# Performance work log

Hardware: AMD Instinct MI355X
Metric: run time of the kernel (lower is better)

Reference implementation:

```python
import jax, jax.numpy as jnp
import numpy as np

B, T, I, H = 128, 1024, 256, 512


def setup_inputs() -> dict:
    key = jax.random.key(0)
    ks = jax.random.split(key, 7)
    s_in = 1.0 / np.sqrt(I + H)  # torch Linear default init scale
    inp = {
        "x": jax.random.normal(ks[0], (B, T, I), dtype=jnp.float32),
        "Wz": jax.random.uniform(ks[1], (I + H, H), jnp.float32, -s_in, s_in),
        "bz": jax.random.uniform(ks[2], (H,), jnp.float32, -s_in, s_in),
        "Wr": jax.random.uniform(ks[3], (I + H, H), jnp.float32, -s_in, s_in),
        "br": jax.random.uniform(ks[4], (H,), jnp.float32, -s_in, s_in),
        "Wh": jax.random.uniform(ks[5], (I + H, H), jnp.float32, -s_in, s_in),
        "bh": jax.random.uniform(ks[6], (H,), jnp.float32, -s_in, s_in),
    }
    return inp


def reference(x, Wz, bz, Wr, br, Wh, bh):
    # x: [B, T, I]; custom GRU cell, h0 = zeros. Note the (nonstandard)
    # blend h = (1-z)*h + z*h_cand, exactly as in the torch source.
    batch, hidden = x.shape[0], Wz.shape[1]

    def step(h, x_t):
        comb = jnp.concatenate([x_t, h], axis=1)          # [B, I+H]
        z = jax.nn.sigmoid(comb @ Wz + bz)                # [B, H]
        r = jax.nn.sigmoid(comb @ Wr + br)                # [B, H]
        comb2 = jnp.concatenate([x_t, r * h], axis=1)     # [B, I+H]
        h_cand = jnp.tanh(comb2 @ Wh + bh)                # [B, H]
        h_new = (1.0 - z) * h + z * h_cand
        return h_new, h_new

    h0 = jnp.zeros((batch, hidden), dtype=x.dtype)
    _, ys = jax.lax.scan(step, h0, jnp.swapaxes(x, 0, 1))  # ys: [T, B, H]
    return jnp.swapaxes(ys, 0, 1)                          # [B, T, H]
```

## Files before the change

kernel.cpp:

```cpp
#include <hip/hip_runtime.h>
#include <math.h>

#define BB 128
#define TT 1024
#define II 256
#define HH 512
#define KK 768

typedef __attribute__((ext_vector_type(8))) short short8v;
typedef __attribute__((ext_vector_type(4))) float float4v;
typedef __attribute__((ext_vector_type(4))) unsigned int uint4v;

#define BARS_OFF   0
#define BARS_SZ    32768
#define WFRAG_OFF  BARS_SZ
#define WFRAG_SZ   (96 * 24 * 64 * 16)
#define GS_OFF     (WFRAG_OFF + WFRAG_SZ)
#define GS_STRIDE  65536
#define WS_NEED    ((size_t)GS_OFF + 8 * GS_STRIDE)

#define NT_MAIN 320

__device__ __forceinline__ unsigned short bf16_rne(float f) {
    unsigned u = __builtin_bit_cast(unsigned, f);
    unsigned r = u + 0x7FFFu + ((u >> 16) & 1u);
    return (unsigned short)(r >> 16);
}
__device__ __forceinline__ void cp16(void* lds, const void* g) {
    __builtin_amdgcn_global_load_lds(
        (const __attribute__((address_space(1))) unsigned*)g,
        (__attribute__((address_space(3))) unsigned*)lds, 16, 0, 0);
}
__device__ __forceinline__ float sigmoid_fast(float v) {
    return __builtin_amdgcn_rcpf(1.f + __expf(-v));
}
__device__ __forceinline__ float tanh_fast(float v) {
    const float e = __expf(2.f * v);
    return 1.f - 2.f * __builtin_amdgcn_rcpf(e + 1.f);
}

#define MFMA __builtin_amdgcn_mfma_f32_16x16x32_bf16

__global__ void repack_w(const float* __restrict__ Wz, const float* __restrict__ Wr,
                         const float* __restrict__ Wh, short8v* __restrict__ wB) {
    const int ntAll = blockIdx.x;
    const int w = threadIdx.x >> 6, l = threadIdx.x & 63;
    const float* W; int n0;
    if (ntAll < 32)      { W = Wz; n0 = ntAll * 16; }
    else if (ntAll < 64) { W = Wr; n0 = (ntAll - 32) * 16; }
    else                 { W = Wh; n0 = (ntAll - 64) * 16; }
    const int n = n0 + (l & 15);
    for (int kt = w; kt < 24; kt += 4) {
        const int k0 = kt * 32 + (l >> 4) * 8;
        short8v f;
        #pragma unroll
        for (int j = 0; j < 8; ++j)
            f[j] = (short)bf16_rne(W[(size_t)(k0 + j) * HH + n]);
        wB[((size_t)ntAll * 24 + kt) * 64 + l] = f;
    }
}

__global__ __launch_bounds__(NT_MAIN, 1) void gru_mfma(
    const float* __restrict__ x,
    const float* __restrict__ bz, const float* __restrict__ br,
    const float* __restrict__ bh,
    float* __restrict__ out,
    const short8v* __restrict__ wB,
    char* __restrict__ gsBase,
    unsigned* __restrict__ bars)
{
    __shared__ short8v bx1[4][8][64];
    __shared__ short8v bx2[2][8][64];
    __shared__ short8v xF[2][8][64];
    __shared__ float4v red1[4][4][64];
    __shared__ float4v red2[2][4][64];
    __shared__ float rhA[16][33];
    __shared__ float hL[16][33];

    const int tid = threadIdx.x;
    const int w = tid >> 6, l = tid & 63;
    const int g = blockIdx.x & 7, s = blockIdx.x >> 3;
    const int m_ = l & 15, kg = l >> 4;

    char* gs = gsBase + (size_t)g * GS_STRIDE;
    short8v* hFrag  = (short8v*)gs;
    short8v* rhFrag = hFrag + 16 * 64;
    unsigned* flagBase = bars + (size_t)g * 16 * 64;

    short8v wh1[4][4];
    short8v wh2[2][4];
    if (w < 4) {
        const int ownNt = (w < 2) ? (2 * s + w) : (32 + 2 * s + (w - 2));
        for (int i = 0; i < 8; ++i)
            cp16(&bx1[w][i][0], wB + ((size_t)ownNt * 24 + i) * 64 + l);
        if (w < 2)
            for (int i = 0; i < 8; ++i)
                cp16(&bx2[w][i][0], wB + ((size_t)(64 + 2 * s + w) * 24 + i) * 64 + l);
        #pragma unroll
        for (int T = 0; T < 4; ++T) {
            const int nt = (T < 2) ? (2 * s + T) : (32 + 2 * s + (T - 2));
            #pragma unroll
            for (int q = 0; q < 4; ++q)
                wh1[T][q] = wB[((size_t)nt * 24 + 8 + 4 * w + q) * 64 + l];
        }
        #pragma unroll
        for (int n2 = 0; n2 < 2; ++n2)
            #pragma unroll
            for (int q = 0; q < 4; ++q)
                wh2[n2][q] = wB[((size_t)(64 + 2 * s + n2) * 24 + 8 + 4 * w + q) * 64 + l];
    }
    const float bias1 = (w < 2) ? bz[s * 32 + w * 16 + m_]
                    : (w < 4)  ? br[s * 32 + (w - 2) * 16 + m_] : 0.f;
    const float bias2 = (w < 2) ? bh[s * 32 + w * 16 + m_] : 0.f;

    for (int idx = tid; idx < 16 * 33; idx += NT_MAIN) ((float*)hL)[idx] = 0.f;

    for (int slot = tid; slot < 512; slot += NT_MAIN) {
        const int kt = slot >> 6, ll = slot & 63;
        const float* xp = x + (size_t)(g * 16 + (ll & 15)) * (TT * II)
                            + kt * 32 + (ll >> 4) * 8;
        const float4 v0 = *(const float4*)xp;
        const float4 v1 = *(const float4*)(xp + 4);
        short8v f;
        f[0] = (short)bf16_rne(v0.x); f[1] = (short)bf16_rne(v0.y);
        f[2] = (short)bf16_rne(v0.z); f[3] = (short)bf16_rne(v0.w);
        f[4] = (short)bf16_rne(v1.x); f[5] = (short)bf16_rne(v1.y);
        f[6] = (short)bf16_rne(v1.z); f[7] = (short)bf16_rne(v1.w);
        xF[0][kt][ll] = f;
    }
    __syncthreads();

    float4 xv[16];

    for (int t = 0; t < TT; ++t) {
        const int xb = t & 1;

        float4v ax0 = {0.f, 0.f, 0.f, 0.f}, ax1 = ax0;
        if (w < 4) {
            #pragma unroll
            for (int kt = 0; kt < 8; kt += 2) {
                ax0 = MFMA(xF[xb][kt][l],     bx1[w][kt][l],     ax0, 0, 0, 0);
                ax1 = MFMA(xF[xb][kt + 1][l], bx1[w][kt + 1][l], ax1, 0, 0, 0);
            }
        } else if (t + 1 < TT) {
            #pragma unroll
            for (int i = 0; i < 8; ++i) {
                const float* xp = x + (size_t)(g * 16 + m_) * (TT * II)
                                    + (size_t)(t + 1) * II + i * 32 + kg * 8;
                xv[2 * i]     = *(const float4*)xp;
                xv[2 * i + 1] = *(const float4*)(xp + 4);
            }
        }

        if (w < 4) {
            if (l < 8) {
                const unsigned* fp = flagBase + (4 * w + (l >> 1)) * 64 + (l & 1) * 8;
                while (__hip_atomic_load(fp, __ATOMIC_RELAXED,
                                         __HIP_MEMORY_SCOPE_AGENT) < (unsigned)t)
                    __builtin_amdgcn_s_sleep(1);
            }
            uint4v u0, u1, u2, u3;
            const short8v* hp = hFrag + (size_t)(4 * w) * 64 + l;
            asm volatile("global_load_dwordx4 %0, %1, off sc1" : "=v"(u0) : "v"(hp)       : "memory");
            asm volatile("global_load_dwordx4 %0, %1, off sc1" : "=v"(u1) : "v"(hp +  64) : "memory");
            asm volatile("global_load_dwordx4 %0, %1, off sc1" : "=v"(u2) : "v"(hp + 128) : "memory");
            asm volatile("global_load_dwordx4 %0, %1, off sc1" : "=v"(u3) : "v"(hp + 192) : "memory");
            asm volatile("s_waitcnt vmcnt(0)" ::: "memory");
            __builtin_amdgcn_sched_barrier(0);
            const short8v hf0 = __builtin_bit_cast(short8v, u0);
            const short8v hf1 = __builtin_bit_cast(short8v, u1);
            const short8v hf2 = __builtin_bit_cast(short8v, u2);
            const short8v hf3 = __builtin_bit_cast(short8v, u3);
            float4v h0 = {0.f,0.f,0.f,0.f}, h1 = h0, h2 = h0, h3 = h0;
            #pragma unroll
            for (int q = 0; q < 4; ++q) {
                const short8v a = (q == 0) ? hf0 : (q == 1) ? hf1 : (q == 2) ? hf2 : hf3;
                h0 = MFMA(a, wh1[0][q], h0, 0, 0, 0);
                h1 = MFMA(a, wh1[1][q], h1, 0, 0, 0);
                h2 = MFMA(a, wh1[2][q], h2, 0, 0, 0);
                h3 = MFMA(a, wh1[3][q], h3, 0, 0, 0);
            }
            red1[0][w][l] = h0; red1[1][w][l] = h1;
            red1[2][w][l] = h2; red1[3][w][l] = h3;
        }
        __syncthreads();

        float zreg[4];
        if (w < 4) {
            float4v s1v = ax0 + ax1 + red1[w][0][l] + red1[w][1][l]
                                  + red1[w][2][l] + red1[w][3][l];
            #pragma unroll
            for (int r = 0; r < 4; ++r) {
                const float sg = sigmoid_fast(s1v[r] + bias1);
                if (w < 2) zreg[r] = sg;
                else rhA[kg * 4 + r][(w - 2) * 16 + m_] =
                         sg * hL[kg * 4 + r][(w - 2) * 16 + m_];
            }
        }
        if (w == 2 || w == 3) {
            asm volatile("s_waitcnt lgkmcnt(0)" ::: "memory");
            __builtin_amdgcn_sched_barrier(0);
            const bool mine = (w == 2) ? (l < 32) : (l >= 32);
            if (mine) {
                short8v f;
                #pragma unroll
                for (int j = 0; j < 8; ++j)
                    f[j] = (short)bf16_rne(rhA[m_][kg * 8 + j]);
                const uint4v u = __builtin_bit_cast(uint4v, f);
                short8v* dp = rhFrag + (size_t)s * 64 + l;
                asm volatile("global_store_dwordx4 %0, %1, off sc1" :: "v"(dp), "v"(u) : "memory");
            }
            asm volatile("s_waitcnt vmcnt(0)" ::: "memory");
            if (w == 2 && l == 0)
                __hip_atomic_store(flagBase + s * 64 + 16, (unsigned)(t + 1),
                                   __ATOMIC_RELAXED, __HIP_MEMORY_SCOPE_AGENT);
            if (w == 3 && l == 32)
                __hip_atomic_store(flagBase + s * 64 + 24, (unsigned)(t + 1),
                                   __ATOMIC_RELAXED, __HIP_MEMORY_SCOPE_AGENT);
        }
        if (w == 4) {
            asm volatile("s_waitcnt vmcnt(0)" ::: "memory");
            if (t + 1 < TT) {
                #pragma unroll
                for (int i = 0; i < 8; ++i) {
                    const float4 v0 = xv[2 * i], v1 = xv[2 * i + 1];
                    short8v f;
                    f[0] = (short)bf16_rne(v0.x); f[1] = (short)bf16_rne(v0.y);
                    f[2] = (short)bf16_rne(v0.z); f[3] = (short)bf16_rne(v0.w);
                    f[4] = (short)bf16_rne(v1.x); f[5] = (short)bf16_rne(v1.y);
                    f[6] = (short)bf16_rne(v1.z); f[7] = (short)bf16_rne(v1.w);
                    xF[xb ^ 1][i][l] = f;
                }
            }
            if (t > 0) {
                float* op = out + (size_t)(g * 16 + m_) * (TT * HH)
                                + (size_t)(t - 1) * HH + s * 32 + kg * 8;
                float4 o0, o1;
                o0.x = hL[m_][kg * 8 + 0]; o0.y = hL[m_][kg * 8 + 1];
                o0.z = hL[m_][kg * 8 + 2]; o0.w = hL[m_][kg * 8 + 3];
                o1.x = hL[m_][kg * 8 + 4]; o1.y = hL[m_][kg * 8 + 5];
                o1.z = hL[m_][kg * 8 + 6]; o1.w = hL[m_][kg * 8 + 7];
                *(float4*)op = o0;
                *(float4*)(op + 4) = o1;
            }
        }

        float4v cx0 = {0.f,0.f,0.f,0.f}, cx1 = cx0;
        if (w < 2) {
            #pragma unroll
            for (int kt = 0; kt < 8; kt += 2) {
                cx0 = MFMA(xF[xb][kt][l],     bx2[w][kt][l],     cx0, 0, 0, 0);
                cx1 = MFMA(xF[xb][kt + 1][l], bx2[w][kt + 1][l], cx1, 0, 0, 0);
            }
        }

        if (w < 4) {
            if (l < 8) {
                const unsigned* fp = flagBase + (4 * w + (l >> 1)) * 64 + 16 + (l & 1) * 8;
                while (__hip_atomic_load(fp, __ATOMIC_RELAXED,
                                         __HIP_MEMORY_SCOPE_AGENT) < (unsigned)(t + 1))
                    __builtin_amdgcn_s_sleep(1);
            }
            uint4v u0, u1, u2, u3;
            const short8v* rp = rhFrag + (size_t)(4 * w) * 64 + l;
            asm volatile("global_load_dwordx4 %0, %1, off sc1" : "=v"(u0) : "v"(rp)       : "memory");
            asm volatile("global_load_dwordx4 %0, %1, off sc1" : "=v"(u1) : "v"(rp +  64) : "memory");
            asm volatile("global_load_dwordx4 %0, %1, off sc1" : "=v"(u2) : "v"(rp + 128) : "memory");
            asm volatile("global_load_dwordx4 %0, %1, off sc1" : "=v"(u3) : "v"(rp + 192) : "memory");
            asm volatile("s_waitcnt vmcnt(0)" ::: "memory");
            __builtin_amdgcn_sched_barrier(0);
            const short8v rf0 = __builtin_bit_cast(short8v, u0);
            const short8v rf1 = __builtin_bit_cast(short8v, u1);
            const short8v rf2 = __builtin_bit_cast(short8v, u2);
            const short8v rf3 = __builtin_bit_cast(short8v, u3);
            float4v c0 = {0.f,0.f,0.f,0.f}, c1 = c0;
            #pragma unroll
            for (int q = 0; q < 4; ++q) {
                const short8v a = (q == 0) ? rf0 : (q == 1) ? rf1 : (q == 2) ? rf2 : rf3;
                c0 = MFMA(a, wh2[0][q], c0, 0, 0, 0);
                c1 = MFMA(a, wh2[1][q], c1, 0, 0, 0);
            }
            red2[0][w][l] = c0; red2[1][w][l] = c1;
        }
        __syncthreads();

        if (w < 2) {
            float4v s2v = cx0 + cx1 + red2[w][0][l] + red2[w][1][l]
                                  + red2[w][2][l] + red2[w][3][l];
            #pragma unroll
            for (int r = 0; r < 4; ++r) {
                const int row = kg * 4 + r;
                const int cl = w * 16 + m_;
                const float hc = tanh_fast(s2v[r] + bias2);
                const float ho = hL[row][cl];
                hL[row][cl] = (1.f - zreg[r]) * ho + zreg[r] * hc;
            }
            asm volatile("s_waitcnt lgkmcnt(0)" ::: "memory");
            __builtin_amdgcn_sched_barrier(0);
            const bool mine = (w == 0) ? (l < 32) : (l >= 32);
            if (mine) {
                short8v f;
                #pragma unroll
                for (int j = 0; j < 8; ++j)
                    f[j] = (short)bf16_rne(hL[m_][kg * 8 + j]);
                const uint4v u = __builtin_bit_cast(uint4v, f);
                short8v* dp = hFrag + (size_t)s * 64 + l;
                asm volatile("global_store_dwordx4 %0, %1, off sc1" :: "v"(dp), "v"(u) : "memory");
            }
            asm volatile("s_waitcnt vmcnt(0)" ::: "memory");
            if (w == 0 && l == 0)
                __hip_atomic_store(flagBase + s * 64 + 0, (unsigned)(t + 1),
                                   __ATOMIC_RELAXED, __HIP_MEMORY_SCOPE_AGENT);
            if (w == 1 && l == 32)
                __hip_atomic_store(flagBase + s * 64 + 8, (unsigned)(t + 1),
                                   __ATOMIC_RELAXED, __HIP_MEMORY_SCOPE_AGENT);
        }
    }

    __syncthreads();
    if (w == 4) {
        float* op = out + (size_t)(g * 16 + m_) * (TT * HH)
                        + (size_t)(TT - 1) * HH + s * 32 + kg * 8;
        float4 o0, o1;
        o0.x = hL[m_][kg * 8 + 0]; o0.y = hL[m_][kg * 8 + 1];
        o0.z = hL[m_][kg * 8 + 2]; o0.w = hL[m_][kg * 8 + 3];
        o1.x = hL[m_][kg * 8 + 4]; o1.y = hL[m_][kg * 8 + 5];
        o1.z = hL[m_][kg * 8 + 6]; o1.w = hL[m_][kg * 8 + 7];
        *(float4*)op = o0;
        *(float4*)(op + 4) = o1;
    }
}

#define NWG_FB 64
#define NTHR_FB 512
__global__ __launch_bounds__(NTHR_FB, 1) void gru_rowsplit(
    const float* __restrict__ x,
    const float* __restrict__ Wz, const float* __restrict__ bz,
    const float* __restrict__ Wr, const float* __restrict__ br,
    const float* __restrict__ Wh, const float* __restrict__ bh,
    float* __restrict__ out)
{
    __shared__ float comb_i [KK][2];
    __shared__ float comb2_i[KK][2];
    __shared__ float z_s[2][HH];
    __shared__ float red1[8][257];
    __shared__ float red2[24][129];

    const int tid  = threadIdx.x;
    const int row0 = blockIdx.x * 2;
    const int kh = tid >> 8;
    const int t1 = tid & 255;
    const int n1 = t1 * 4;
    const float* __restrict__ w1 =
        ((n1 < HH) ? (Wz + n1) : (Wr + (n1 - HH))) + (size_t)(kh * 384) * HH;
    const int kq = tid >> 7;
    const int t2 = tid & 127;
    const int n2 = t2 * 4;
    const float* __restrict__ w2 = Wh + n2 + (size_t)(kq * 192) * HH;

    float b1[4], b2[4];
    #pragma unroll
    for (int j = 0; j < 4; ++j) {
        b1[j] = (n1 + j < HH) ? bz[n1 + j] : br[n1 + j - HH];
        b2[j] = bh[n2 + j];
    }
    for (int idx = tid; idx < HH * 2; idx += NTHR_FB)
        comb_i[II + (idx >> 1)][idx & 1] = 0.f;
    __syncthreads();

    for (int t = 0; t < TT; ++t) {
        {
            const int r = tid >> 8, k = tid & 255;
            const float v = x[(size_t)(row0 + r) * (TT * II) + (size_t)t * II + k];
            comb_i [k][r] = v;
            comb2_i[k][r] = v;
        }
        __syncthreads();
        float a00=0,a01=0,a02=0,a03=0,a10=0,a11=0,a12=0,a13=0;
        {
            const int kb = kh * 384;
            #pragma unroll 8
            for (int k = 0; k < 384; ++k) {
                const float4 w = *(const float4*)(w1 + (size_t)k * HH);
                const float2 a = *(const float2*)&comb_i[kb + k][0];
                a00 += a.x*w.x; a01 += a.x*w.y; a02 += a.x*w.z; a03 += a.x*w.w;
                a10 += a.y*w.x; a11 += a.y*w.y; a12 += a.y*w.z; a13 += a.y*w.w;
            }
        }
        if (kh == 1) {
            red1[0][t1]=a00; red1[1][t1]=a01; red1[2][t1]=a02; red1[3][t1]=a03;
            red1[4][t1]=a10; red1[5][t1]=a11; red1[6][t1]=a12; red1[7][t1]=a13;
        }
        __syncthreads();
        if (kh == 0) {
            float accv[2][4] = {{a00,a01,a02,a03},{a10,a11,a12,a13}};
            #pragma unroll
            for (int r = 0; r < 2; ++r) {
                #pragma unroll
                for (int j = 0; j < 4; ++j) {
                    const int n = n1 + j;
                    const float v = accv[r][j] + red1[r*4+j][t1] + b1[j];
                    const float sg = 1.f / (1.f + __expf(-v));
                    if (n < HH) z_s[r][n] = sg;
                    else {
                        const int nh = n - HH;
                        comb2_i[II + nh][r] = sg * comb_i[II + nh][r];
                    }
                }
            }
        }
        __syncthreads();
        float c00=0,c01=0,c02=0,c03=0,c10=0,c11=0,c12=0,c13=0;
        {
            const int kb = kq * 192;
            #pragma unroll 8
            for (int k = 0; k < 192; ++k) {
                const float4 w = *(const float4*)(w2 + (size_t)k * HH);
                const float2 a = *(const float2*)&comb2_i[kb + k][0];
                c00 += a.x*w.x; c01 += a.x*w.y; c02 += a.x*w.z; c03 += a.x*w.w;
                c10 += a.y*w.x; c11 += a.y*w.y; c12 += a.y*w.z; c13 += a.y*w.w;
            }
        }
        if (kq > 0) {
            const int base = (kq - 1) * 8;
            red2[base+0][t2]=c00; red2[base+1][t2]=c01;
            red2[base+2][t2]=c02; red2[base+3][t2]=c03;
            red2[base+4][t2]=c10; red2[base+5][t2]=c11;
            red2[base+6][t2]=c12; red2[base+7][t2]=c13;
        }
        __syncthreads();
        if (kq == 0) {
            float accv[2][4] = {{c00,c01,c02,c03},{c10,c11,c12,c13}};
            #pragma unroll
            for (int r = 0; r < 2; ++r) {
                float hn4[4];
                #pragma unroll
                for (int j = 0; j < 4; ++j) {
                    const int n = n2 + j;
                    const int jj = r * 4 + j;
                    const float v = accv[r][j] + red2[jj][t2] + red2[8+jj][t2]
                                  + red2[16+jj][t2] + b2[j];
                    const float hc = tanhf(v);
                    const float zv = z_s[r][n];
                    const float ho = comb_i[II + n][r];
                    const float hn = (1.f - zv) * ho + zv * hc;
                    comb_i[II + n][r] = hn;
                    hn4[j] = hn;
                }
                *(float4*)&out[(size_t)(row0 + r) * (TT * HH) + (size_t)t * HH + n2] =
                    make_float4(hn4[0], hn4[1], hn4[2], hn4[3]);
            }
        }
        __syncthreads();
    }
}

extern "C" void kernel_launch(void* const* d_in, const int* in_sizes, int n_in,
                              void* d_out, int out_size, void* d_ws, size_t ws_size,
                              hipStream_t stream) {
    const float* x  = (const float*)d_in[0];
    const float* Wz = (const float*)d_in[1];
    const float* bz = (const float*)d_in[2];
    const float* Wr = (const float*)d_in[3];
    const float* br = (const float*)d_in[4];
    const float* Wh = (const float*)d_in[5];
    const float* bh = (const float*)d_in[6];
    float* out = (float*)d_out;

    if (ws_size < WS_NEED) {
        gru_rowsplit<<<NWG_FB, NTHR_FB, 0, stream>>>(x, Wz, bz, Wr, br, Wh, bh, out);
        return;
    }

    char* ws = (char*)d_ws;
    unsigned* bars = (unsigned*)(ws + BARS_OFF);
    short8v*  wB   = (short8v*)(ws + WFRAG_OFF);
    char*     gs   = ws + GS_OFF;

    hipMemsetAsync(bars, 0, BARS_SZ, stream);
    hipMemsetAsync(gs, 0, 8 * (size_t)GS_STRIDE, stream);
    repack_w<<<96, 256, 0, stream>>>(Wz, Wr, Wh, wB);
    gru_mfma<<<128, NT_MAIN, 0, stream>>>(x, bz, br, bh, out, wB, gs, bars);
}
```

Baseline: 4.569 ms.

## Probe at runtime for shared-L2 locality and use sc0 cache-scope polling when safe

Adds a startup probe in which the 16 workgroups of each batch group exchange flags using sc0-scoped loads and stores, checking whether they can see each other's writes. If every member of the group passes, the per-step flag polling, fragment stores and fragment loads switch from sc1 (device-scope) to sc0 cache policy and spin without s_sleep. The goal is lower latency on the two cross-workgroup exchanges in every timestep. It risks relying on coherence behaviour that only the probe confirms, which could go wrong if workgroups land on different XCDs. It also adds probe setup cost and doubles the barrier workspace.

```diff
diff --git a/kernel.cpp b/kernel.cpp
--- a/kernel.cpp
+++ b/kernel.cpp
@@ -12,7 +12,7 @@
 typedef __attribute__((ext_vector_type(4))) unsigned int uint4v;
 
 #define BARS_OFF   0
-#define BARS_SZ    32768
+#define BARS_SZ    65536
 #define WFRAG_OFF  BARS_SZ
 #define WFRAG_SZ   (96 * 24 * 64 * 16)
 #define GS_OFF     (WFRAG_OFF + WFRAG_SZ)
@@ -37,6 +37,22 @@
 __device__ __forceinline__ float tanh_fast(float v) {
     const float e = __expf(2.f * v);
     return 1.f - 2.f * __builtin_amdgcn_rcpf(e + 1.f);
+}
+__device__ __forceinline__ unsigned poll_ld(const unsigned* p, bool fast) {
+    unsigned v;
+    if (fast) asm volatile("global_load_dword %0, %1, off sc0\n\ts_waitcnt vmcnt(0)"
+                           : "=v"(v) : "v"(p) : "memory");
+    else      asm volatile("global_load_dword %0, %1, off sc1\n\ts_waitcnt vmcnt(0)"
+                           : "=v"(v) : "v"(p) : "memory");
+    return v;
+}
+__device__ __forceinline__ void frag_st16(void* p, uint4v u, bool fast) {
+    if (fast) asm volatile("global_store_dwordx4 %0, %1, off sc0" :: "v"(p), "v"(u) : "memory");
+    else      asm volatile("global_store_dwordx4 %0, %1, off sc1" :: "v"(p), "v"(u) : "memory");
+}
+__device__ __forceinline__ void flag_pub(unsigned* p, unsigned v, bool fast) {
+    if (fast) asm volatile("global_store_dword %0, %1, off sc0" :: "v"(p), "v"(v) : "memory");
+    else      __hip_atomic_store(p, v, __ATOMIC_RELAXED, __HIP_MEMORY_SCOPE_AGENT);
 }
 
 #define MFMA __builtin_amdgcn_mfma_f32_16x16x32_bf16
@@ -76,6 +92,7 @@
     __shared__ float4v red2[2][4][64];
     __shared__ float rhA[16][33];
     __shared__ float hL[16][33];
+    __shared__ int fastSh;
 
     const int tid = threadIdx.x;
     const int w = tid >> 6, l = tid & 63;
@@ -85,7 +102,8 @@
     char* gs = gsBase + (size_t)g * GS_STRIDE;
     short8v* hFrag  = (short8v*)gs;
     short8v* rhFrag = hFrag + 16 * 64;
-    unsigned* flagBase = bars + (size_t)g * 16 * 64;
+    unsigned* flagBase  = bars + (size_t)g * 16 * 64;
+    unsigned* probeBase = bars + 8192 + (size_t)g * 16 * 64;
 
     short8v wh1[4][4];
     short8v wh2[2][4];
@@ -115,6 +133,45 @@
 
     for (int idx = tid; idx < 16 * 33; idx += NT_MAIN) ((float*)hL)[idx] = 0.f;
 
+    if (w == 0) {
+        int okAll = 1;
+        for (int round = 1; round <= 4; ++round) {
+            if (l == 0) {
+                unsigned* pp = probeBase + s * 64;
+                asm volatile("global_store_dword %0, %1, off sc0\n\ts_waitcnt vmcnt(0)"
+                             :: "v"(pp), "v"((unsigned)round) : "memory");
+            }
+            bool seen = (l >= 16);
+            if (l < 16) {
+                const unsigned* pp = probeBase + l * 64;
+                const unsigned bound = (round == 1) ? 8192u : 2048u;
+                for (unsigned it = 0; it < bound; ++it) {
+                    unsigned v;
+                    asm volatile("global_load_dword %0, %1, off sc0\n\ts_waitcnt vmcnt(0)"
+                                 : "=v"(v) : "v"(pp) : "memory");
+                    if (v >= (unsigned)round) { seen = true; break; }
+                }
+            }
+            okAll &= (((unsigned long long)__ballot(seen) & 0xFFFFull) == 0xFFFFull) ? 1 : 0;
+        }
+        if (l == 0)
+            __hip_atomic_store(probeBase + s * 64 + 16, (unsigned)(1 + okAll),
+                               __ATOMIC_RELAXED, __HIP_MEMORY_SCOPE_AGENT);
+        bool good = (l >= 16);
+        if (l < 16) {
+            const unsigned* vp = probeBase + l * 64 + 16;
+            unsigned v;
+            for (;;) {
+                v = __hip_atomic_load(vp, __ATOMIC_RELAXED, __HIP_MEMORY_SCOPE_AGENT);
+                if (v != 0u) break;
+                __builtin_amdgcn_s_sleep(1);
+            }
+            good = (v == 2u);
+        }
+        if (l == 0)
+            fastSh = (((unsigned long long)__ballot(good) & 0xFFFFull) == 0xFFFFull) ? 1 : 0;
+    }
+
     for (int slot = tid; slot < 512; slot += NT_MAIN) {
         const int kt = slot >> 6, ll = slot & 63;
         const float* xp = x + (size_t)(g * 16 + (ll & 15)) * (TT * II)
@@ -129,6 +186,7 @@
         xF[0][kt][ll] = f;
     }
     __syncthreads();
+    const bool fast = (fastSh != 0);
 
     float4 xv[16];
 
@@ -155,16 +213,26 @@
         if (w < 4) {
             if (l < 8) {
                 const unsigned* fp = flagBase + (4 * w + (l >> 1)) * 64 + (l & 1) * 8;
-                while (__hip_atomic_load(fp, __ATOMIC_RELAXED,
-                                         __HIP_MEMORY_SCOPE_AGENT) < (unsigned)t)
-                    __builtin_amdgcn_s_sleep(1);
+                if (fast) { while (poll_ld(fp, true) < (unsigned)t) {} }
+                else {
+                    while (__hip_atomic_load(fp, __ATOMIC_RELAXED,
+                                             __HIP_MEMORY_SCOPE_AGENT) < (unsigned)t)
+                        __builtin_amdgcn_s_sleep(1);
+                }
             }
             uint4v u0, u1, u2, u3;
             const short8v* hp = hFrag + (size_t)(4 * w) * 64 + l;
-            asm volatile("global_load_dwordx4 %0, %1, off sc1" : "=v"(u0) : "v"(hp)       : "memory");
-            asm volatile("global_load_dwordx4 %0, %1, off sc1" : "=v"(u1) : "v"(hp +  64) : "memory");
-            asm volatile("global_load_dwordx4 %0, %1, off sc1" : "=v"(u2) : "v"(hp + 128) : "memory");
-            asm volatile("global_load_dwordx4 %0, %1, off sc1" : "=v"(u3) : "v"(hp + 192) : "memory");
+            if (fast) {
+                asm volatile("global_load_dwordx4 %0, %1, off sc0" : "=v"(u0) : "v"(hp)       : "memory");
+                asm volatile("global_load_dwordx4 %0, %1, off sc0" : "=v"(u1) : "v"(hp +  64) : "memory");
+                asm volatile("global_load_dwordx4 %0, %1, off sc0" : "=v"(u2) : "v"(hp + 128) : "memory");
+                asm volatile("global_load_dwordx4 %0, %1, off sc0" : "=v"(u3) : "v"(hp + 192) : "memory");
+            } else {
+                asm volatile("global_load_dwordx4 %0, %1, off sc1" : "=v"(u0) : "v"(hp)       : "memory");
+                asm volatile("global_load_dwordx4 %0, %1, off sc1" : "=v"(u1) : "v"(hp +  64) : "memory");
+                asm volatile("global_load_dwordx4 %0, %1, off sc1" : "=v"(u2) : "v"(hp + 128) : "memory");
+                asm volatile("global_load_dwordx4 %0, %1, off sc1" : "=v"(u3) : "v"(hp + 192) : "memory");
+            }
             asm volatile("s_waitcnt vmcnt(0)" ::: "memory");
             __builtin_amdgcn_sched_barrier(0);
             const short8v hf0 = __builtin_bit_cast(short8v, u0);
@@ -206,17 +274,11 @@
                 #pragma unroll
                 for (int j = 0; j < 8; ++j)
                     f[j] = (short)bf16_rne(rhA[m_][kg * 8 + j]);
-                const uint4v u = __builtin_bit_cast(uint4v, f);
-                short8v* dp = rhFrag + (size_t)s * 64 + l;
-                asm volatile("global_store_dwordx4 %0, %1, off sc1" :: "v"(dp), "v"(u) : "memory");
+                frag_st16(rhFrag + (size_t)s * 64 + l, __builtin_bit_cast(uint4v, f), fast);
             }
             asm volatile("s_waitcnt vmcnt(0)" ::: "memory");
-            if (w == 2 && l == 0)
-                __hip_atomic_store(flagBase + s * 64 + 16, (unsigned)(t + 1),
-                                   __ATOMIC_RELAXED, __HIP_MEMORY_SCOPE_AGENT);
-            if (w == 3 && l == 32)
-                __hip_atomic_store(flagBase + s * 64 + 24, (unsigned)(t + 1),
-                                   __ATOMIC_RELAXED, __HIP_MEMORY_SCOPE_AGENT);
+            if (w == 2 && l == 0)  flag_pub(flagBase + s * 64 + 16, (unsigned)(t + 1), fast);
+            if (w == 3 && l == 32) flag_pub(flagBase + s * 64 + 24, (unsigned)(t + 1), fast);
         }
         if (w == 4) {
             asm volatile("s_waitcnt vmcnt(0)" ::: "memory");
@@ -257,16 +319,26 @@
         if (w < 4) {
             if (l < 8) {
                 const unsigned* fp = flagBase + (4 * w + (l >> 1)) * 64 + 16 + (l & 1) * 8;
-                while (__hip_atomic_load(fp, __ATOMIC_RELAXED,
-                                         __HIP_MEMORY_SCOPE_AGENT) < (unsigned)(t + 1))
-                    __builtin_amdgcn_s_sleep(1);
+                if (fast) { while (poll_ld(fp, true) < (unsigned)(t + 1)) {} }
+                else {
+                    while (__hip_atomic_load(fp, __ATOMIC_RELAXED,
+                                             __HIP_MEMORY_SCOPE_AGENT) < (unsigned)(t + 1))
+                        __builtin_amdgcn_s_sleep(1);
+                }
             }
             uint4v u0, u1, u2, u3;
             const short8v* rp = rhFrag + (size_t)(4 * w) * 64 + l;
-            asm volatile("global_load_dwordx4 %0, %1, off sc1" : "=v"(u0) : "v"(rp)       : "memory");
-            asm volatile("global_load_dwordx4 %0, %1, off sc1" : "=v"(u1) : "v"(rp +  64) : "memory");
-            asm volatile("global_load_dwordx4 %0, %1, off sc1" : "=v"(u2) : "v"(rp + 128) : "memory");
-            asm volatile("global_load_dwordx4 %0, %1, off sc1" : "=v"(u3) : "v"(rp + 192) : "memory");
+            if (fast) {
+                asm volatile("global_load_dwordx4 %0, %1, off sc0" : "=v"(u0) : "v"(rp)       : "memory");
+                asm volatile("global_load_dwordx4 %0, %1, off sc0" : "=v"(u1) : "v"(rp +  64) : "memory");
+                asm volatile("global_load_dwordx4 %0, %1, off sc0" : "=v"(u2) : "v"(rp + 128) : "memory");
+                asm volatile("global_load_dwordx4 %0, %1, off sc0" : "=v"(u3) : "v"(rp + 192) : "memory");
+            } else {
+                asm volatile("global_load_dwordx4 %0, %1, off sc1" : "=v"(u0) : "v"(rp)       : "memory");
+                asm volatile("global_load_dwordx4 %0, %1, off sc1" : "=v"(u1) : "v"(rp +  64) : "memory");
+                asm volatile("global_load_dwordx4 %0, %1, off sc1" : "=v"(u2) : "v"(rp + 128) : "memory");
+                asm volatile("global_load_dwordx4 %0, %1, off sc1" : "=v"(u3) : "v"(rp + 192) : "memory");
+            }
             asm volatile("s_waitcnt vmcnt(0)" ::: "memory");
             __builtin_amdgcn_sched_barrier(0);
             const short8v rf0 = __builtin_bit_cast(short8v, u0);
@@ -303,17 +375,11 @@
                 #pragma unroll
                 for (int j = 0; j < 8; ++j)
                     f[j] = (short)bf16_rne(hL[m_][kg * 8 + j]);
-                const uint4v u = __builtin_bit_cast(uint4v, f);
-                short8v* dp = hFrag + (size_t)s * 64 + l;
-                asm volatile("global_store_dwordx4 %0, %1, off sc1" :: "v"(dp), "v"(u) : "memory");
+                frag_st16(hFrag + (size_t)s * 64 + l, __builtin_bit_cast(uint4v, f), fast);
             }
             asm volatile("s_waitcnt vmcnt(0)" ::: "memory");
-            if (w == 0 && l == 0)
-                __hip_atomic_store(flagBase + s * 64 + 0, (unsigned)(t + 1),
-                                   __ATOMIC_RELAXED, __HIP_MEMORY_SCOPE_AGENT);
-            if (w == 1 && l == 32)
-                __hip_atomic_store(flagBase + s * 64 + 8, (unsigned)(t + 1),
-                                   __ATOMIC_RELAXED, __HIP_MEMORY_SCOPE_AGENT);
+            if (w == 0 && l == 0)  flag_pub(flagBase + s * 64 + 0, (unsigned)(t + 1), fast);
+            if (w == 1 && l == 32) flag_pub(flagBase + s * 64 + 8, (unsigned)(t + 1), fast);
         }
     }
 
```

New measurement: 5.544 ms. 1.21x slower.

## Replace flag-based cross-block sync with epoch-tagged data messages

Applied to the files above, without the earlier changes.

Each published bf16 pair of the h and r*h fragments now carries its own epoch word in an 8-byte store. Consumers poll the data itself until every epoch reaches the step, which removes the separate flag arrays, the store-then-wait-then-flag sequence, and the flag spin loop. This cuts one global round trip per exchange. In exchange, message traffic doubles, each poll issues sixteen dwordx2 loads, and correctness relies on each 8-byte store being seen atomically.

```diff
diff --git a/kernel.cpp b/kernel.cpp
--- a/kernel.cpp
+++ b/kernel.cpp
@@ -10,12 +10,11 @@
 typedef __attribute__((ext_vector_type(8))) short short8v;
 typedef __attribute__((ext_vector_type(4))) float float4v;
 typedef __attribute__((ext_vector_type(4))) unsigned int uint4v;
-
-#define BARS_OFF   0
-#define BARS_SZ    32768
-#define WFRAG_OFF  BARS_SZ
+typedef __attribute__((ext_vector_type(2))) unsigned int uint2v;
+
+#define WFRAG_OFF  0
 #define WFRAG_SZ   (96 * 24 * 64 * 16)
-#define GS_OFF     (WFRAG_OFF + WFRAG_SZ)
+#define GS_OFF     WFRAG_SZ
 #define GS_STRIDE  65536
 #define WS_NEED    ((size_t)GS_OFF + 8 * GS_STRIDE)
 
@@ -38,6 +37,7 @@
     const float e = __expf(2.f * v);
     return 1.f - 2.f * __builtin_amdgcn_rcpf(e + 1.f);
 }
+__device__ __forceinline__ unsigned umin2(unsigned a, unsigned b) { return a < b ? a : b; }
 
 #define MFMA __builtin_amdgcn_mfma_f32_16x16x32_bf16
 
@@ -66,8 +66,7 @@
     const float* __restrict__ bh,
     float* __restrict__ out,
     const short8v* __restrict__ wB,
-    char* __restrict__ gsBase,
-    unsigned* __restrict__ bars)
+    char* __restrict__ gsBase)
 {
     __shared__ short8v bx1[4][8][64];
     __shared__ short8v bx2[2][8][64];
@@ -83,9 +82,8 @@
     const int m_ = l & 15, kg = l >> 4;
 
     char* gs = gsBase + (size_t)g * GS_STRIDE;
-    short8v* hFrag  = (short8v*)gs;
-    short8v* rhFrag = hFrag + 16 * 64;
-    unsigned* flagBase = bars + (size_t)g * 16 * 64;
+    char* hMsg  = gs;
+    char* rhMsg = gs + 32768;
 
     short8v wh1[4][4];
     short8v wh2[2][4];
@@ -115,6 +113,13 @@
 
     for (int idx = tid; idx < 16 * 33; idx += NT_MAIN) ((float*)hL)[idx] = 0.f;
 
+    const char* hA0 = hMsg  + (size_t)(4 * w) * 2048 + (size_t)l * 32;
+    const char* hA1 = hA0 + 4096;
+    const char* rA0 = rhMsg + (size_t)(4 * w) * 2048 + (size_t)l * 32;
+    const char* rA1 = rA0 + 4096;
+    char* hPub  = hMsg  + (size_t)s * 2048 + (size_t)l * 32;
+    char* rhPub = rhMsg + (size_t)s * 2048 + (size_t)l * 32;
+
     for (int slot = tid; slot < 512; slot += NT_MAIN) {
         const int kt = slot >> 6, ll = slot & 63;
         const float* xp = x + (size_t)(g * 16 + (ll & 15)) * (TT * II)
@@ -130,10 +135,70 @@
     }
     __syncthreads();
 
+#define LOADWAIT16(B0, B1)                                                     \
+    asm volatile(                                                              \
+        "global_load_dwordx2 %0, %16, off sc1\n\t"                             \
+        "global_load_dwordx2 %1, %16, off offset:8 sc1\n\t"                    \
+        "global_load_dwordx2 %2, %16, off offset:16 sc1\n\t"                   \
+        "global_load_dwordx2 %3, %16, off offset:24 sc1\n\t"                   \
+        "global_load_dwordx2 %4, %16, off offset:2048 sc1\n\t"                 \
+        "global_load_dwordx2 %5, %16, off offset:2056 sc1\n\t"                 \
+        "global_load_dwordx2 %6, %16, off offset:2064 sc1\n\t"                 \
+        "global_load_dwordx2 %7, %16, off offset:2072 sc1\n\t"                 \
+        "global_load_dwordx2 %8, %17, off sc1\n\t"                             \
+        "global_load_dwordx2 %9, %17, off offset:8 sc1\n\t"                    \
+        "global_load_dwordx2 %10, %17, off offset:16 sc1\n\t"                  \
+        "global_load_dwordx2 %11, %17, off offset:24 sc1\n\t"                  \
+        "global_load_dwordx2 %12, %17, off offset:2048 sc1\n\t"                \
+        "global_load_dwordx2 %13, %17, off offset:2056 sc1\n\t"                \
+        "global_load_dwordx2 %14, %17, off offset:2064 sc1\n\t"                \
+        "global_load_dwordx2 %15, %17, off offset:2072 sc1\n\t"                \
+        "s_waitcnt vmcnt(0)"                                                   \
+        : "=&v"(p0), "=&v"(p1), "=&v"(p2), "=&v"(p3),                          \
+          "=&v"(p4), "=&v"(p5), "=&v"(p6), "=&v"(p7),                          \
+          "=&v"(p8), "=&v"(p9), "=&v"(p10), "=&v"(p11),                        \
+          "=&v"(p12), "=&v"(p13), "=&v"(p14), "=&v"(p15)                       \
+        : "v"(B0), "v"(B1)                                                     \
+        : "memory")
+
+#define EPOCH_MIN()                                                            \
+    umin2(umin2(umin2(umin2(p0[1], p1[1]), umin2(p2[1], p3[1])),               \
+                umin2(umin2(p4[1], p5[1]), umin2(p6[1], p7[1]))),              \
+          umin2(umin2(umin2(p8[1], p9[1]), umin2(p10[1], p11[1])),             \
+                umin2(umin2(p12[1], p13[1]), umin2(p14[1], p15[1]))))
+
+#define PUB4(SRC, DST, EPOCH)                                                                   \
+    do {                                                                                        \
+        uint2v u;                                                                               \
+        u[1] = (EPOCH);                                                                         \
+        u[0] = (unsigned)bf16_rne(SRC[m_][kg * 8 + 0]) | ((unsigned)bf16_rne(SRC[m_][kg * 8 + 1]) << 16); \
+        asm volatile("global_store_dwordx2 %0, %1, off sc1" :: "v"(DST), "v"(u) : "memory");    \
+        u[0] = (unsigned)bf16_rne(SRC[m_][kg * 8 + 2]) | ((unsigned)bf16_rne(SRC[m_][kg * 8 + 3]) << 16); \
+        asm volatile("global_store_dwordx2 %0, %1, off offset:8 sc1" :: "v"(DST), "v"(u) : "memory");  \
+        u[0] = (unsigned)bf16_rne(SRC[m_][kg * 8 + 4]) | ((unsigned)bf16_rne(SRC[m_][kg * 8 + 5]) << 16); \
+        asm volatile("global_store_dwordx2 %0, %1, off offset:16 sc1" :: "v"(DST), "v"(u) : "memory"); \
+        u[0] = (unsigned)bf16_rne(SRC[m_][kg * 8 + 6]) | ((unsigned)bf16_rne(SRC[m_][kg * 8 + 7]) << 16); \
+        asm volatile("global_store_dwordx2 %0, %1, off offset:24 sc1" :: "v"(DST), "v"(u) : "memory"); \
+    } while (0)
+
+#define ASSEMBLE4(F0, F1, F2, F3)                                              \
+    do {                                                                       \
+        uint4v a;                                                              \
+        a[0] = p0[0];  a[1] = p1[0];  a[2] = p2[0];  a[3] = p3[0];             \
+        F0 = __builtin_bit_cast(short8v, a);                                   \
+        a[0] = p4[0];  a[1] = p5[0];  a[2] = p6[0];  a[3] = p7[0];             \
+        F1 = __builtin_bit_cast(short8v, a);                                   \
+        a[0] = p8[0];  a[1] = p9[0];  a[2] = p10[0]; a[3] = p11[0];            \
+        F2 = __builtin_bit_cast(short8v, a);                                   \
+        a[0] = p12[0]; a[1] = p13[0]; a[2] = p14[0]; a[3] = p15[0];            \
+        F3 = __builtin_bit_cast(short8v, a);                                   \
+    } while (0)
+
     float4 xv[16];
 
     for (int t = 0; t < TT; ++t) {
         const int xb = t & 1;
+        uint2v p0, p1, p2, p3, p4, p5, p6, p7, p8, p9, p10, p11, p12, p13, p14, p15;
 
         float4v ax0 = {0.f, 0.f, 0.f, 0.f}, ax1 = ax0;
         if (w < 4) {
@@ -142,6 +207,24 @@
                 ax0 = MFMA(xF[xb][kt][l],     bx1[w][kt][l],     ax0, 0, 0, 0);
                 ax1 = MFMA(xF[xb][kt + 1][l], bx1[w][kt + 1][l], ax1, 0, 0, 0);
             }
+            for (;;) {
+                LOADWAIT16(hA0, hA1);
+                if (__all((int)(EPOCH_MIN() >= (unsigned)t))) break;
+            }
+            __builtin_amdgcn_sched_barrier(0);
+            short8v hf0, hf1, hf2, hf3;
+            ASSEMBLE4(hf0, hf1, hf2, hf3);
+            float4v h0 = {0.f,0.f,0.f,0.f}, h1 = h0, h2 = h0, h3 = h0;
+            #pragma unroll
+            for (int q = 0; q < 4; ++q) {
+                const short8v aq = (q == 0) ? hf0 : (q == 1) ? hf1 : (q == 2) ? hf2 : hf3;
+                h0 = MFMA(aq, wh1[0][q], h0, 0, 0, 0);
+                h1 = MFMA(aq, wh1[1][q], h1, 0, 0, 0);
+                h2 = MFMA(aq, wh1[2][q], h2, 0, 0, 0);
+                h3 = MFMA(aq, wh1[3][q], h3, 0, 0, 0);
+            }
+            red1[0][w][l] = h0; red1[1][w][l] = h1;
+            red1[2][w][l] = h2; red1[3][w][l] = h3;
         } else if (t + 1 < TT) {
             #pragma unroll
             for (int i = 0; i < 8; ++i) {
@@ -151,38 +234,6 @@
                 xv[2 * i + 1] = *(const float4*)(xp + 4);
             }
         }
-
-        if (w < 4) {
-            if (l < 8) {
-                const unsigned* fp = flagBase + (4 * w + (l >> 1)) * 64 + (l & 1) * 8;
-                while (__hip_atomic_load(fp, __ATOMIC_RELAXED,
-                                         __HIP_MEMORY_SCOPE_AGENT) < (unsigned)t)
-                    __builtin_amdgcn_s_sleep(1);
-            }
-            uint4v u0, u1, u2, u3;
-            const short8v* hp = hFrag + (size_t)(4 * w) * 64 + l;
-            asm volatile("global_load_dwordx4 %0, %1, off sc1" : "=v"(u0) : "v"(hp)       : "memory");
-            asm volatile("global_load_dwordx4 %0, %1, off sc1" : "=v"(u1) : "v"(hp +  64) : "memory");
-            asm volatile("global_load_dwordx4 %0, %1, off sc1" : "=v"(u2) : "v"(hp + 128) : "memory");
-            asm volatile("global_load_dwordx4 %0, %1, off sc1" : "=v"(u3) : "v"(hp + 192) : "memory");
-            asm volatile("s_waitcnt vmcnt(0)" ::: "memory");
-            __builtin_amdgcn_sched_barrier(0);
-            const short8v hf0 = __builtin_bit_cast(short8v, u0);
-            const short8v hf1 = __builtin_bit_cast(short8v, u1);
-            const short8v hf2 = __builtin_bit_cast(short8v, u2);
-            const short8v hf3 = __builtin_bit_cast(short8v, u3);
-            float4v h0 = {0.f,0.f,0.f,0.f}, h1 = h0, h2 = h0, h3 = h0;
-            #pragma unroll
-            for (int q = 0; q < 4; ++q) {
-                const short8v a = (q == 0) ? hf0 : (q == 1) ? hf1 : (q == 2) ? hf2 : hf3;
-                h0 = MFMA(a, wh1[0][q], h0, 0, 0, 0);
-                h1 = MFMA(a, wh1[1][q], h1, 0, 0, 0);
-                h2 = MFMA(a, wh1[2][q], h2, 0, 0, 0);
-                h3 = MFMA(a, wh1[3][q], h3, 0, 0, 0);
-            }
-            red1[0][w][l] = h0; red1[1][w][l] = h1;
-            red1[2][w][l] = h2; red1[3][w][l] = h3;
-        }
         __syncthreads();
 
         float zreg[4];
@@ -201,22 +252,7 @@
             asm volatile("s_waitcnt lgkmcnt(0)" ::: "memory");
             __builtin_amdgcn_sched_barrier(0);
             const bool mine = (w == 2) ? (l < 32) : (l >= 32);
-            if (mine) {
-                short8v f;
-                #pragma unroll
-                for (int j = 0; j < 8; ++j)
-                    f[j] = (short)bf16_rne(rhA[m_][kg * 8 + j]);
-                const uint4v u = __builtin_bit_cast(uint4v, f);
-                short8v* dp = rhFrag + (size_t)s * 64 + l;
-                asm volatile("global_store_dwordx4 %0, %1, off sc1" :: "v"(dp), "v"(u) : "memory");
-            }
-            asm volatile("s_waitcnt vmcnt(0)" ::: "memory");
-            if (w == 2 && l == 0)
-                __hip_atomic_store(flagBase + s * 64 + 16, (unsigned)(t + 1),
-                                   __ATOMIC_RELAXED, __HIP_MEMORY_SCOPE_AGENT);
-            if (w == 3 && l == 32)
-                __hip_atomic_store(flagBase + s * 64 + 24, (unsigned)(t + 1),
-                                   __ATOMIC_RELAXED, __HIP_MEMORY_SCOPE_AGENT);
+            if (mine) { PUB4(rhA, rhPub, (unsigned)(t + 1)); }
         }
         if (w == 4) {
             asm volatile("s_waitcnt vmcnt(0)" ::: "memory");
@@ -253,34 +289,23 @@
                 cx1 = MFMA(xF[xb][kt + 1][l], bx2[w][kt + 1][l], cx1, 0, 0, 0);
             }
         }
-
         if (w < 4) {
-            if (l < 8) {
-                const unsigned* fp = flagBase + (4 * w + (l >> 1)) * 64 + 16 + (l & 1) * 8;
-                while (__hip_atomic_load(fp, __ATOMIC_RELAXED,
-                                         __HIP_MEMORY_SCOPE_AGENT) < (unsigned)(t + 1))
-                    __builtin_amdgcn_s_sleep(1);
-            }
-            uint4v u0, u1, u2, u3;
-            const short8v* rp = rhFrag + (size_t)(4 * w) * 64 + l;
-            asm volatile("global_load_dwordx4 %0, %1, off sc1" : "=v"(u0) : "v"(rp)       : "memory");
-            asm volatile("global_load_dwordx4 %0, %1, off sc1" : "=v"(u1) : "v"(rp +  64) : "memory");
-            asm volatile("global_load_dwordx4 %0, %1, off sc1" : "=v"(u2) : "v"(rp + 128) : "memory");
-            asm volatile("global_load_dwordx4 %0, %1, off sc1" : "=v"(u3) : "v"(rp + 192) : "memory");
-            asm volatile("s_waitcnt vmcnt(0)" ::: "memory");
+            for (;;) {
+                LOADWAIT16(rA0, rA1);
+                if (__all((int)(EPOCH_MIN() >= (unsigned)(t + 1)))) break;
+            }
             __builtin_amdgcn_sched_barrier(0);
-            const short8v rf0 = __builtin_bit_cast(short8v, u0);
-            const short8v rf1 = __builtin_bit_cast(short8v, u1);
-            const short8v rf2 = __builtin_bit_cast(short8v, u2);
-            const short8v rf3 = __builtin_bit_cast(short8v, u3);
+            short8v rf0, rf1, rf2, rf3;
+            ASSEMBLE4(rf0, rf1, rf2, rf3);
             float4v c0 = {0.f,0.f,0.f,0.f}, c1 = c0;
             #pragma unroll
             for (int q = 0; q < 4; ++q) {
-                const short8v a = (q == 0) ? rf0 : (q == 1) ? rf1 : (q == 2) ? rf2 : rf3;
-                c0 = MFMA(a, wh2[0][q], c0, 0, 0, 0);
-                c1 = MFMA(a, wh2[1][q], c1, 0, 0, 0);
-            }
-            red2[0][w][l] = c0; red2[1][w][l] = c1;
+                const short8v aq = (q == 0) ? rf0 : (q == 1) ? rf1 : (q == 2) ? rf2 : rf3;
+                c0 = MFMA(aq, wh2[0][q], c0, 0, 0, 0);
+                c1 = MFMA(aq, wh2[1][q], c1, 0, 0, 0);
+            }
+            red2[0][w][l] = c0;
+            red2[1][w][l] = c1;
         }
         __syncthreads();
 
@@ -298,24 +323,13 @@
             asm volatile("s_waitcnt lgkmcnt(0)" ::: "memory");
             __builtin_amdgcn_sched_barrier(0);
             const bool mine = (w == 0) ? (l < 32) : (l >= 32);
-            if (mine) {
-                short8v f;
-                #pragma unroll
-                for (int j = 0; j < 8; ++j)
-                    f[j] = (short)bf16_rne(hL[m_][kg * 8 + j]);
-                const uint4v u = __builtin_bit_cast(uint4v, f);
-                short8v* dp = hFrag + (size_t)s * 64 + l;
-                asm volatile("global_store_dwordx4 %0, %1, off sc1" :: "v"(dp), "v"(u) : "memory");
-            }
-            asm volatile("s_waitcnt vmcnt(0)" ::: "memory");
-            if (w == 0 && l == 0)
-                __hip_atomic_store(flagBase + s * 64 + 0, (unsigned)(t + 1),
-                                   __ATOMIC_RELAXED, __HIP_MEMORY_SCOPE_AGENT);
-            if (w == 1 && l == 32)
-                __hip_atomic_store(flagBase + s * 64 + 8, (unsigned)(t + 1),
-                                   __ATOMIC_RELAXED, __HIP_MEMORY_SCOPE_AGENT);
-        }
-    }
+            if (mine) { PUB4(hL, hPub, (unsigned)(t + 1)); }
+        }
+    }
+#undef LOADWAIT16
+#undef EPOCH_MIN
+#undef PUB4
+#undef ASSEMBLE4
 
     __syncthreads();
     if (w == 4) {
@@ -473,12 +487,10 @@
     }
 
     char* ws = (char*)d_ws;
-    unsigned* bars = (unsigned*)(ws + BARS_OFF);
-    short8v*  wB   = (short8v*)(ws + WFRAG_OFF);
-    char*     gs   = ws + GS_OFF;
-
-    hipMemsetAsync(bars, 0, BARS_SZ, stream);
+    short8v* wB = (short8v*)(ws + WFRAG_OFF);
+    char*    gs = ws + GS_OFF;
+
     hipMemsetAsync(gs, 0, 8 * (size_t)GS_STRIDE, stream);
     repack_w<<<96, 256, 0, stream>>>(Wz, Wr, Wh, wB);
-    gru_mfma<<<128, NT_MAIN, 0, stream>>>(x, bz, br, bh, out, wB, gs, bars);
-}
+    gru_mfma<<<128, NT_MAIN, 0, stream>>>(x, bz, br, bh, out, wB, gs);
+}
```

After: 12.08 ms. 2.64x slower.
